# Kernel optimization log

Measured on AMD Instinct MI355X. Metric: run time of the kernel, lower is better.

Reference implementation:

```python
import jax, jax.numpy as jnp
import numpy as np

C_IN, SEQ_LEN, N_KERNELS, KSS, KS_MAX, BATCH = 1, 512, 1000, [7, 9, 11], 11, 64


def setup_inputs() -> dict:
    rng = np.random.default_rng(0)
    ks_l, dil_l, pad_l, lout_l = [], [], [], []
    W = np.zeros((N_KERNELS, C_IN, KS_MAX), dtype=np.float32)
    for k in range(N_KERNELS):
        ks = int(rng.choice(KSS))
        d_f = 2.0 ** rng.uniform(0.0, np.log2((SEQ_LEN - 1) // (ks - 1)))
        pad = int((ks - 1) * d_f // 2) if rng.integers(2) == 1 else 0
        d = int(d_f)
        # torch passes padding=2*pad to Conv1d -> adds 2*pad on EACH side
        lout = SEQ_LEN + 4 * pad - d * (ks - 1)
        w = rng.standard_normal((1, C_IN, ks)).astype(np.float32)
        w -= w.mean()  # center like the original (global mean)
        W[k, :, :ks] = w[0]
        ks_l.append(ks); dil_l.append(d); pad_l.append(pad); lout_l.append(lout)
    dils = np.asarray(dil_l, dtype=np.int64)
    pads = np.asarray(pad_l, dtype=np.int64)
    l_out = np.asarray(lout_l, dtype=np.int32)
    max_L = int(l_out.max())
    t = np.arange(max_L)
    j = np.arange(KS_MAX)
    # raw input index for output position t, tap j of kernel k
    raw = t[None, None, :] - 2 * pads[:, None, None] + j[None, :, None] * dils[:, None, None]
    valid = (raw >= 0) & (raw < SEQ_LEN)  # zero-padding semantics
    idx = np.clip(raw, 0, SEQ_LEN - 1).astype(np.int32)
    bias = (2.0 * (rng.random(N_KERNELS) - 0.5)).astype(np.float32)
    key = jax.random.key(0)
    x = jax.random.normal(key, (BATCH, C_IN, SEQ_LEN), dtype=jnp.float32)
    return {
        "x": x,
        "weight": jnp.asarray(W),
        "bias": jnp.asarray(bias),
        "idx": jnp.asarray(idx),
        "valid": jnp.asarray(valid),
        "l_out": jnp.asarray(l_out),
    }


def _forward(x, weight, bias, idx, valid, l_out):
    B = x.shape[0]
    K, C, KS = weight.shape
    L = idx.shape[-1]
    validf = valid.astype(x.dtype)  # [K, KS, L]
    acc = jnp.zeros((B, K, L), dtype=x.dtype)
    for j in range(KS):  # fixed small tap loop; each kernel vectorized over K
        xg = x[:, :, idx[:, j, :]]  # [B, C, K, L] gather along time
        acc = acc + jnp.einsum("bckt,kc->bkt", xg, weight[:, :, j]) * validf[None, :, j, :]
    out = acc + bias[None, :, None]  # [B, K, L]
    tmask = jnp.arange(L)[None, :] < l_out[:, None]  # [K, L] valid output positions
    neg = jnp.finfo(x.dtype).min
    mx = jnp.max(jnp.where(tmask[None], out, neg), axis=-1)  # [B, K]
    ppv = jnp.sum(jnp.where(tmask[None] & (out > 0), 1.0, 0.0), axis=-1) / l_out.astype(x.dtype)[None]
    # torch interleaves [max_i, ppv_i] along dim=1
    return jnp.stack([mx, ppv], axis=-1).reshape(B, 2 * K)


def reference(x, weight, bias, idx, valid, l_out):
    return _forward(x, weight, bias, idx, valid, l_out)
```

## Files before the change

### kernel.cpp

```cpp
#include <hip/hip_runtime.h>
#include <hip/hip_fp16.h>
#include <float.h>

constexpr int KMAX  = 11;
constexpr int SEQ   = 512;
constexpr int NB    = 64;
constexpr int NBB   = 8;
constexpr int NGRP  = NB / NBB;
constexpr int MSTR  = 32;
constexpr int WSLOT = 1600;

__device__ __forceinline__ unsigned h2b(__half2 h) { unsigned u; __builtin_memcpy(&u, &h, 4); return u; }
__device__ __forceinline__ __half2  b2h(unsigned u) { __half2 h; __builtin_memcpy(&h, &u, 4); return h; }

__device__ __forceinline__ unsigned pkmax(unsigned a, unsigned b) {
    unsigned d; asm("v_pk_max_f16 %0, %1, %2" : "=v"(d) : "v"(a), "v"(b)); return d;
}
__device__ __forceinline__ unsigned pkadd(unsigned a, unsigned b) { return h2b(__hadd2(b2h(a), b2h(b))); }
__device__ __forceinline__ __half2 h2max(__half2 a, __half2 b) { return b2h(pkmax(h2b(a), h2b(b))); }
__device__ __forceinline__ unsigned pkfma_clamp(unsigned a, unsigned b, unsigned c) {
    unsigned d; asm("v_pk_fma_f16 %0, %1, %2, %3 clamp" : "=v"(d) : "v"(a), "v"(b), "v"(c)); return d;
}

template<int CTRL>
__device__ __forceinline__ unsigned dppmov(unsigned old, unsigned v) {
    return (unsigned)__builtin_amdgcn_update_dpp((int)old, (int)v, CTRL, 0xF, 0xF, false);
}
constexpr unsigned NEGINF2 = 0xFC00FC00u;

__device__ __forceinline__ unsigned dpp_redmax(unsigned x) {
    x = pkmax(x, dppmov<0xB1 >(NEGINF2, x));
    x = pkmax(x, dppmov<0x4E >(NEGINF2, x));
    x = pkmax(x, dppmov<0x141>(NEGINF2, x));
    x = pkmax(x, dppmov<0x140>(NEGINF2, x));
    x = pkmax(x, dppmov<0x142>(NEGINF2, x));
    x = pkmax(x, dppmov<0x143>(NEGINF2, x));
    return x;
}
__device__ __forceinline__ unsigned dpp_redadd(unsigned x) {
    x = pkadd(x, dppmov<0xB1 >(0u, x));
    x = pkadd(x, dppmov<0x4E >(0u, x));
    x = pkadd(x, dppmov<0x141>(0u, x));
    x = pkadd(x, dppmov<0x140>(0u, x));
    x = pkadd(x, dppmov<0x142>(0u, x));
    x = pkadd(x, dppmov<0x143>(0u, x));
    return x;
}

__global__ __launch_bounds__(256)
void prep_kernel(const float* __restrict__ x, const float* __restrict__ w,
                 const int* __restrict__ idx, int* __restrict__ meta,
                 unsigned short* __restrict__ xt, int K, int maxL)
{
    const int tid = threadIdx.x;
    if ((int)blockIdx.x >= K) {
        const int j  = ((int)blockIdx.x - K) * 256 + tid;
        const int b  = j >> 7;
        const int s4 = j & 127;
        const float4 v = reinterpret_cast<const float4*>(x)[b * (SEQ / 4) + s4];
        const int g = b >> 3, bl = b & 7;
        unsigned short* dst = xt + ((size_t)g * SEQ + s4 * 4) * NBB + bl;
        __half h;
        h = __float2half_rn(v.x); __builtin_memcpy(&dst[0 * NBB], &h, 2);
        h = __float2half_rn(v.y); __builtin_memcpy(&dst[1 * NBB], &h, 2);
        h = __float2half_rn(v.z); __builtin_memcpy(&dst[2 * NBB], &h, 2);
        h = __float2half_rn(v.w); __builtin_memcpy(&dst[3 * NBB], &h, 2);
        return;
    }

    __shared__ int c_sh[KMAX];
    const int k = blockIdx.x, wave = tid >> 6, lane = tid & 63;

    for (int j = wave; j < KMAX; j += 4) {
        const int* row = idx + ((size_t)k * KMAX + j) * (size_t)maxL;
        int c = 0;
        for (int base = 0; base < maxL; base += 64) {
            const int t = base + lane;
            const int v = (t < maxL) ? row[t] : 0;
            const bool interior = (v > 0) && (v < SEQ - 1);
            const unsigned long long mb = __ballot(interior);
            if (mb != 0ull) {
                const int fl = __builtin_ctzll(mb);
                c = __shfl(v, fl) - (base + fl);
                break;
            }
        }
        if (lane == 0) c_sh[j] = c;
    }
    __syncthreads();

    if (tid == 0) {
        int* mk = meta + (size_t)k * MSTR;
        int n = 0, cmin = 0, cmax = 0;
        for (int j = 0; j < KMAX; ++j) {
            const float wj = w[(size_t)k * KMAX + j];
            if (wj != 0.0f) {
                const int c = c_sh[j];
                mk[1 + n] = c;
                __half hw = __float2half_rn(wj);
                unsigned short ub; __builtin_memcpy(&ub, &hw, 2);
                mk[12 + n] = (unsigned)ub | ((unsigned)ub << 16);
                cmin = min(cmin, c); cmax = max(cmax, c);
                ++n;
            }
        }
        for (int jj = n; jj < KMAX; ++jj) { mk[1 + jj] = 0; mk[12 + jj] = 0; }
        mk[0]  = n;
        mk[23] = cmin;
        mk[24] = cmax;
    }
}

template<int NJ>
__device__ __forceinline__ void conv_body(
    const char* __restrict__ xsc, const int* __restrict__ msh,
    int lout, int x0, int wave, int lane, unsigned ctermb,
    __half2 (&mx2)[4], __half2 (&ct2)[4])
{
    const __half2 zero2 = __float2half2_rn(0.f);
    const __half2 nbig2 = __float2half2_rn(-65504.f);
    const unsigned C4b  = 0x74007400u;

    int addr[NJ]; __half2 wr[NJ];
#pragma unroll
    for (int j = 0; j < NJ; ++j) {
        const int c = __builtin_amdgcn_readfirstlane(msh[1 + j]);
        wr[j]   = b2h((unsigned)__builtin_amdgcn_readfirstlane(msh[12 + j]));
        addr[j] = (wave * 64 + lane + c + x0) * 16;
    }
#pragma unroll
    for (int m = 0; m < 4; ++m) { mx2[m] = nbig2; ct2[m] = zero2; }

#pragma unroll
    for (int it = 0; it < 4; ++it) {
        const int tb = wave * 64 + it * 256;
        if (tb + 64 <= lout) {
            uint4 d[NJ];
#pragma unroll
            for (int j = 0; j < NJ; ++j)
                d[j] = *reinterpret_cast<const uint4*>(xsc + addr[j] + it * 4096);
            __half2 a[4] = {zero2, zero2, zero2, zero2};
#pragma unroll
            for (int j = 0; j < NJ; ++j) {
                a[0] = __hfma2(wr[j], b2h(d[j].x), a[0]);
                a[1] = __hfma2(wr[j], b2h(d[j].y), a[1]);
                a[2] = __hfma2(wr[j], b2h(d[j].z), a[2]);
                a[3] = __hfma2(wr[j], b2h(d[j].w), a[3]);
            }
#pragma unroll
            for (int m = 0; m < 4; ++m) {
                mx2[m] = h2max(mx2[m], a[m]);
                ct2[m] = b2h(pkadd(h2b(ct2[m]), pkfma_clamp(h2b(a[m]), C4b, ctermb)));
            }
        }
    }

    const int rem = lout & 63;
    if (rem) {
        const int pc = lout >> 6;
        if ((pc & 3) == wave) {
            const int off = (pc >> 2) << 12;
            uint4 d[NJ];
#pragma unroll
            for (int j = 0; j < NJ; ++j)
                d[j] = *reinterpret_cast<const uint4*>(xsc + addr[j] + off);
            __half2 a[4] = {zero2, zero2, zero2, zero2};
#pragma unroll
            for (int j = 0; j < NJ; ++j) {
                a[0] = __hfma2(wr[j], b2h(d[j].x), a[0]);
                a[1] = __hfma2(wr[j], b2h(d[j].y), a[1]);
                a[2] = __hfma2(wr[j], b2h(d[j].z), a[2]);
                a[3] = __hfma2(wr[j], b2h(d[j].w), a[3]);
            }
            const bool tm = lane < rem;
#pragma unroll
            for (int m = 0; m < 4; ++m) {
                a[m] = tm ? a[m] : nbig2;
                mx2[m] = h2max(mx2[m], a[m]);
                ct2[m] = b2h(pkadd(h2b(ct2[m]), pkfma_clamp(h2b(a[m]), C4b, ctermb)));
            }
        }
    }
}

__global__ __launch_bounds__(256, 4)
void rocket_main(const unsigned short* __restrict__ xt, const int* __restrict__ meta,
                 const float* __restrict__ bias, const int* __restrict__ l_out,
                 float* __restrict__ out, int K)
{
    __shared__ __align__(16) unsigned xs_u[WSLOT * 4];
    __shared__ unsigned redm[4][4], redc[4][4];
    __shared__ int msh[MSTR];

    const int k    = blockIdx.x;
    const int grp  = blockIdx.y;
    const int tid  = threadIdx.x;
    const int wave = __builtin_amdgcn_readfirstlane(tid >> 6);
    const int lane = tid & 63;

    if (tid < MSTR) msh[tid] = meta[(size_t)k * MSTR + tid];
    __syncthreads();

    const int   x0    = -msh[23];
    const int   lout  = l_out[k];
    const float biasf = bias[k];
    const int   uend  = min(WSLOT, lout + 63 + msh[24] + x0 + 1);

    float4* xs4 = reinterpret_cast<float4*>(xs_u);
    const float4 z4 = make_float4(0.f, 0.f, 0.f, 0.f);
    for (int i = tid; i < x0; i += 256) xs4[i] = z4;
    for (int i = x0 + SEQ + tid; i < uend; i += 256) xs4[i] = z4;
    const float4* src = reinterpret_cast<const float4*>(xt + (size_t)grp * SEQ * NBB);
    xs4[x0 + tid]       = src[tid];
    xs4[x0 + 256 + tid] = src[256 + tid];
    __syncthreads();

    const int      nj     = __builtin_amdgcn_readfirstlane(msh[0]);
    const unsigned ctermb = h2b(__float2half2_rn(biasf * 16384.f));

    __half2 mx2[4], ct2[4];
    const char* xsc = reinterpret_cast<const char*>(xs_u);
    if (nj <= 7)      conv_body<7 >(xsc, msh, lout, x0, wave, lane, ctermb, mx2, ct2);
    else if (nj <= 9) conv_body<9 >(xsc, msh, lout, x0, wave, lane, ctermb, mx2, ct2);
    else              conv_body<11>(xsc, msh, lout, x0, wave, lane, ctermb, mx2, ct2);

    unsigned um[4], uc[4];
#pragma unroll
    for (int m = 0; m < 4; ++m) {
        um[m] = dpp_redmax(h2b(mx2[m]));
        uc[m] = dpp_redadd(h2b(ct2[m]));
    }
    if (lane == 63) {
#pragma unroll
        for (int m = 0; m < 4; ++m) { redm[wave][m] = um[m]; redc[wave][m] = uc[m]; }
    }
    __syncthreads();

    if (tid < 16) {
        const int bl = tid >> 1, kind = tid & 1;
        const int m = bl >> 1, hi = bl & 1;
        const int b = grp * NBB + bl;
        if (kind == 0) {
            float v = -FLT_MAX;
#pragma unroll
            for (int wv = 0; wv < 4; ++wv) {
                const __half2 h = b2h(redm[wv][m]);
                v = fmaxf(v, hi ? __high2float(h) : __low2float(h));
            }
            out[(size_t)b * (2 * K) + 2 * k] = v + biasf;
        } else {
            float s = 0.f;
#pragma unroll
            for (int wv = 0; wv < 4; ++wv) {
                const __half2 h = b2h(redc[wv][m]);
                s += hi ? __high2float(h) : __low2float(h);
            }
            out[(size_t)b * (2 * K) + 2 * k + 1] = s / (float)lout;
        }
    }
}

extern "C" void kernel_launch(void* const* d_in, const int* in_sizes, int n_in,
                              void* d_out, int out_size, void* d_ws, size_t ws_size,
                              hipStream_t stream)
{
    const float* x    = (const float*)d_in[0];
    const float* w    = (const float*)d_in[1];
    const float* bias = (const float*)d_in[2];
    const int*   idx  = (const int*)d_in[3];
    const int*   lout = (const int*)d_in[5];
    float* out = (float*)d_out;

    const int K    = in_sizes[2];
    const int maxL = in_sizes[3] / (K * KMAX);

    int* meta = (int*)d_ws;
    size_t meta_bytes = ((size_t)K * MSTR * sizeof(int) + 255) & ~(size_t)255;
    unsigned short* xt = (unsigned short*)((char*)d_ws + meta_bytes);

    prep_kernel<<<K + 32, 256, 0, stream>>>(x, w, idx, meta, xt, K, maxL);
    rocket_main<<<dim3(K, NGRP), 256, 0, stream>>>(xt, meta, bias, lout, out, K);
}
```

Measured before the change: 34.27 us.

## Assign one kernel per wave and share a fixed-offset LDS tile across four kernels

Each block now handles four convolution kernels, one per wave, instead of splitting one kernel's output positions across four waves. The input tile is staged once into LDS at a fixed base offset and reused by all four waves, which removes the per-kernel offset metadata and the cross-wave LDS reduction with its extra barrier. Each wave walks all of its output positions alone and writes its results directly. The risk is load imbalance between waves whose kernels have different output lengths and tap counts, plus longer serial loops per wave and a quarter as many blocks.

```diff
diff --git a/kernel.cpp b/kernel.cpp
--- a/kernel.cpp
+++ b/kernel.cpp
@@ -7,7 +7,9 @@
 constexpr int NB    = 64;
 constexpr int NBB   = 8;
 constexpr int NGRP  = NB / NBB;
+constexpr int KPB   = 4;
 constexpr int MSTR  = 32;
+constexpr int SBASE = 512;
 constexpr int WSLOT = 1600;
 
 __device__ __forceinline__ unsigned h2b(__half2 h) { unsigned u; __builtin_memcpy(&u, &h, 4); return u; }
@@ -55,8 +57,7 @@
     const int tid = threadIdx.x;
     if ((int)blockIdx.x >= K) {
         const int j  = ((int)blockIdx.x - K) * 256 + tid;
-        const int b  = j >> 7;
-        const int s4 = j & 127;
+        const int b  = j >> 7, s4 = j & 127;
         const float4 v = reinterpret_cast<const float4*>(x)[b * (SEQ / 4) + s4];
         const int g = b >> 3, bl = b & 7;
         unsigned short* dst = xt + ((size_t)g * SEQ + s4 * 4) * NBB + bl;
@@ -91,31 +92,26 @@
 
     if (tid == 0) {
         int* mk = meta + (size_t)k * MSTR;
-        int n = 0, cmin = 0, cmax = 0;
+        int n = 0;
         for (int j = 0; j < KMAX; ++j) {
             const float wj = w[(size_t)k * KMAX + j];
             if (wj != 0.0f) {
-                const int c = c_sh[j];
-                mk[1 + n] = c;
+                mk[1 + n] = c_sh[j];
                 __half hw = __float2half_rn(wj);
                 unsigned short ub; __builtin_memcpy(&ub, &hw, 2);
                 mk[12 + n] = (unsigned)ub | ((unsigned)ub << 16);
-                cmin = min(cmin, c); cmax = max(cmax, c);
                 ++n;
             }
         }
         for (int jj = n; jj < KMAX; ++jj) { mk[1 + jj] = 0; mk[12 + jj] = 0; }
-        mk[0]  = n;
-        mk[23] = cmin;
-        mk[24] = cmax;
+        mk[0] = n;
     }
 }
 
 template<int NJ>
-__device__ __forceinline__ void conv_body(
-    const char* __restrict__ xsc, const int* __restrict__ msh,
-    int lout, int x0, int wave, int lane, unsigned ctermb,
-    __half2 (&mx2)[4], __half2 (&ct2)[4])
+__device__ __forceinline__ void conv_wave(
+    const char* __restrict__ xsc, int mrow, int lout, int lane, unsigned ctermb,
+    unsigned (&um)[4], unsigned (&uc)[4])
 {
     const __half2 zero2 = __float2half2_rn(0.f);
     const __half2 nbig2 = __float2half2_rn(-65504.f);
@@ -124,21 +120,24 @@
     int addr[NJ]; __half2 wr[NJ];
 #pragma unroll
     for (int j = 0; j < NJ; ++j) {
-        const int c = __builtin_amdgcn_readfirstlane(msh[1 + j]);
-        wr[j]   = b2h((unsigned)__builtin_amdgcn_readfirstlane(msh[12 + j]));
-        addr[j] = (wave * 64 + lane + c + x0) * 16;
-    }
+        const int c = __builtin_amdgcn_readlane(mrow, 1 + j);
+        wr[j]   = b2h((unsigned)__builtin_amdgcn_readlane(mrow, 12 + j));
+        addr[j] = (lane + c + SBASE) * 16;
+    }
+    __half2 mx2[4], ct2[4];
 #pragma unroll
     for (int m = 0; m < 4; ++m) { mx2[m] = nbig2; ct2[m] = zero2; }
 
-#pragma unroll
-    for (int it = 0; it < 4; ++it) {
-        const int tb = wave * 64 + it * 256;
-        if (tb + 64 <= lout) {
+    const int nfull = lout >> 6;
+    const int ng4   = nfull >> 2;
+
+    for (int g = 0; g < ng4; ++g) {
+#pragma unroll
+        for (int u = 0; u < 4; ++u) {
             uint4 d[NJ];
 #pragma unroll
             for (int j = 0; j < NJ; ++j)
-                d[j] = *reinterpret_cast<const uint4*>(xsc + addr[j] + it * 4096);
+                d[j] = *reinterpret_cast<const uint4*>(xsc + addr[j] + u * 1024);
             __half2 a[4] = {zero2, zero2, zero2, zero2};
 #pragma unroll
             for (int j = 0; j < NJ; ++j) {
@@ -153,33 +152,57 @@
                 ct2[m] = b2h(pkadd(h2b(ct2[m]), pkfma_clamp(h2b(a[m]), C4b, ctermb)));
             }
         }
-    }
-
+#pragma unroll
+        for (int j = 0; j < NJ; ++j) addr[j] += 4096;
+    }
+    for (int u = 0; u < (nfull & 3); ++u) {
+        uint4 d[NJ];
+#pragma unroll
+        for (int j = 0; j < NJ; ++j)
+            d[j] = *reinterpret_cast<const uint4*>(xsc + addr[j]);
+        __half2 a[4] = {zero2, zero2, zero2, zero2};
+#pragma unroll
+        for (int j = 0; j < NJ; ++j) {
+            a[0] = __hfma2(wr[j], b2h(d[j].x), a[0]);
+            a[1] = __hfma2(wr[j], b2h(d[j].y), a[1]);
+            a[2] = __hfma2(wr[j], b2h(d[j].z), a[2]);
+            a[3] = __hfma2(wr[j], b2h(d[j].w), a[3]);
+        }
+#pragma unroll
+        for (int m = 0; m < 4; ++m) {
+            mx2[m] = h2max(mx2[m], a[m]);
+            ct2[m] = b2h(pkadd(h2b(ct2[m]), pkfma_clamp(h2b(a[m]), C4b, ctermb)));
+        }
+#pragma unroll
+        for (int j = 0; j < NJ; ++j) addr[j] += 1024;
+    }
     const int rem = lout & 63;
     if (rem) {
-        const int pc = lout >> 6;
-        if ((pc & 3) == wave) {
-            const int off = (pc >> 2) << 12;
-            uint4 d[NJ];
-#pragma unroll
-            for (int j = 0; j < NJ; ++j)
-                d[j] = *reinterpret_cast<const uint4*>(xsc + addr[j] + off);
-            __half2 a[4] = {zero2, zero2, zero2, zero2};
-#pragma unroll
-            for (int j = 0; j < NJ; ++j) {
-                a[0] = __hfma2(wr[j], b2h(d[j].x), a[0]);
-                a[1] = __hfma2(wr[j], b2h(d[j].y), a[1]);
-                a[2] = __hfma2(wr[j], b2h(d[j].z), a[2]);
-                a[3] = __hfma2(wr[j], b2h(d[j].w), a[3]);
-            }
-            const bool tm = lane < rem;
-#pragma unroll
-            for (int m = 0; m < 4; ++m) {
-                a[m] = tm ? a[m] : nbig2;
-                mx2[m] = h2max(mx2[m], a[m]);
-                ct2[m] = b2h(pkadd(h2b(ct2[m]), pkfma_clamp(h2b(a[m]), C4b, ctermb)));
-            }
-        }
+        uint4 d[NJ];
+#pragma unroll
+        for (int j = 0; j < NJ; ++j)
+            d[j] = *reinterpret_cast<const uint4*>(xsc + addr[j]);
+        __half2 a[4] = {zero2, zero2, zero2, zero2};
+#pragma unroll
+        for (int j = 0; j < NJ; ++j) {
+            a[0] = __hfma2(wr[j], b2h(d[j].x), a[0]);
+            a[1] = __hfma2(wr[j], b2h(d[j].y), a[1]);
+            a[2] = __hfma2(wr[j], b2h(d[j].z), a[2]);
+            a[3] = __hfma2(wr[j], b2h(d[j].w), a[3]);
+        }
+        const bool tm = lane < rem;
+#pragma unroll
+        for (int m = 0; m < 4; ++m) {
+            a[m] = tm ? a[m] : nbig2;
+            mx2[m] = h2max(mx2[m], a[m]);
+            ct2[m] = b2h(pkadd(h2b(ct2[m]), pkfma_clamp(h2b(a[m]), C4b, ctermb)));
+        }
+    }
+
+#pragma unroll
+    for (int m = 0; m < 4; ++m) {
+        um[m] = dpp_redmax(h2b(mx2[m]));
+        uc[m] = dpp_redadd(h2b(ct2[m]));
     }
 }
 
@@ -189,73 +212,48 @@
                  float* __restrict__ out, int K)
 {
     __shared__ __align__(16) unsigned xs_u[WSLOT * 4];
-    __shared__ unsigned redm[4][4], redc[4][4];
-    __shared__ int msh[MSTR];
-
-    const int k    = blockIdx.x;
-    const int grp  = blockIdx.y;
-    const int tid  = threadIdx.x;
-    const int wave = __builtin_amdgcn_readfirstlane(tid >> 6);
-    const int lane = tid & 63;
-
-    if (tid < MSTR) msh[tid] = meta[(size_t)k * MSTR + tid];
+
+    const int kbase = (int)blockIdx.x * KPB;
+    const int grp   = blockIdx.y;
+    const int tid   = threadIdx.x;
+    const int wave  = tid >> 6, lane = tid & 63;
+
+    float4* xs4 = reinterpret_cast<float4*>(xs_u);
+    const float4* src = reinterpret_cast<const float4*>(xt + (size_t)grp * SEQ * NBB);
+    const float4 z4 = make_float4(0.f, 0.f, 0.f, 0.f);
+    for (int i = tid; i < WSLOT; i += 256) {
+        const int s = i - SBASE;
+        xs4[i] = ((unsigned)s < (unsigned)SEQ) ? src[s] : z4;
+    }
     __syncthreads();
 
-    const int   x0    = -msh[23];
-    const int   lout  = l_out[k];
-    const float biasf = bias[k];
-    const int   uend  = min(WSLOT, lout + 63 + msh[24] + x0 + 1);
-
-    float4* xs4 = reinterpret_cast<float4*>(xs_u);
-    const float4 z4 = make_float4(0.f, 0.f, 0.f, 0.f);
-    for (int i = tid; i < x0; i += 256) xs4[i] = z4;
-    for (int i = x0 + SEQ + tid; i < uend; i += 256) xs4[i] = z4;
-    const float4* src = reinterpret_cast<const float4*>(xt + (size_t)grp * SEQ * NBB);
-    xs4[x0 + tid]       = src[tid];
-    xs4[x0 + 256 + tid] = src[256 + tid];
-    __syncthreads();
-
-    const int      nj     = __builtin_amdgcn_readfirstlane(msh[0]);
+    const int k = kbase + wave;
+    if (k >= K) return;
+
+    const int mrow  = meta[(size_t)k * MSTR + (lane & 31)];
+    const int nj    = __builtin_amdgcn_readlane(mrow, 0);
+    const int lout  = __builtin_amdgcn_readfirstlane(l_out[k]);
+    const float biasf = __int_as_float(__builtin_amdgcn_readfirstlane(__float_as_int(bias[k])));
     const unsigned ctermb = h2b(__float2half2_rn(biasf * 16384.f));
 
-    __half2 mx2[4], ct2[4];
+    unsigned um[4], uc[4];
     const char* xsc = reinterpret_cast<const char*>(xs_u);
-    if (nj <= 7)      conv_body<7 >(xsc, msh, lout, x0, wave, lane, ctermb, mx2, ct2);
-    else if (nj <= 9) conv_body<9 >(xsc, msh, lout, x0, wave, lane, ctermb, mx2, ct2);
-    else              conv_body<11>(xsc, msh, lout, x0, wave, lane, ctermb, mx2, ct2);
-
-    unsigned um[4], uc[4];
-#pragma unroll
-    for (int m = 0; m < 4; ++m) {
-        um[m] = dpp_redmax(h2b(mx2[m]));
-        uc[m] = dpp_redadd(h2b(ct2[m]));
-    }
+    if (nj <= 7)      conv_wave<7 >(xsc, mrow, lout, lane, ctermb, um, uc);
+    else if (nj <= 9) conv_wave<9 >(xsc, mrow, lout, lane, ctermb, um, uc);
+    else              conv_wave<11>(xsc, mrow, lout, lane, ctermb, um, uc);
+
     if (lane == 63) {
-#pragma unroll
-        for (int m = 0; m < 4; ++m) { redm[wave][m] = um[m]; redc[wave][m] = uc[m]; }
-    }
-    __syncthreads();
-
-    if (tid < 16) {
-        const int bl = tid >> 1, kind = tid & 1;
-        const int m = bl >> 1, hi = bl & 1;
-        const int b = grp * NBB + bl;
-        if (kind == 0) {
-            float v = -FLT_MAX;
-#pragma unroll
-            for (int wv = 0; wv < 4; ++wv) {
-                const __half2 h = b2h(redm[wv][m]);
-                v = fmaxf(v, hi ? __high2float(h) : __low2float(h));
-            }
-            out[(size_t)b * (2 * K) + 2 * k] = v + biasf;
-        } else {
-            float s = 0.f;
-#pragma unroll
-            for (int wv = 0; wv < 4; ++wv) {
-                const __half2 h = b2h(redc[wv][m]);
-                s += hi ? __high2float(h) : __low2float(h);
-            }
-            out[(size_t)b * (2 * K) + 2 * k + 1] = s / (float)lout;
+        const float loutf = (float)lout;
+#pragma unroll
+        for (int m = 0; m < 4; ++m) {
+            const __half2 hm = b2h(um[m]);
+            const __half2 hc = b2h(uc[m]);
+            float* o0 = out + (size_t)(grp * NBB + 2 * m) * (2 * K) + 2 * k;
+            o0[0] = __low2float(hm) + biasf;
+            o0[1] = __low2float(hc) / loutf;
+            float* o1 = o0 + 2 * K;
+            o1[0] = __high2float(hm) + biasf;
+            o1[1] = __high2float(hc) / loutf;
         }
     }
 }
@@ -279,5 +277,5 @@
     unsigned short* xt = (unsigned short*)((char*)d_ws + meta_bytes);
 
     prep_kernel<<<K + 32, 256, 0, stream>>>(x, w, idx, meta, xt, K, maxL);
-    rocket_main<<<dim3(K, NGRP), 256, 0, stream>>>(xt, meta, bias, lout, out, K);
-}
+    rocket_main<<<dim3((K + KPB - 1) / KPB, NGRP), 256, 0, stream>>>(xt, meta, bias, lout, out, K);
+}
```

New measurement: 31.21 us. -8.9%, faster.
